# Performance work log

Hardware: AMD Instinct MI355X
Metric: run time of the kernel (lower is better)

The kernel has to match this reference:

```python
import jax, jax.numpy as jnp
import numpy as np

B, S1, S2, H = 8, 2048, 2048, 1024

def setup_inputs() -> dict:
    key = jax.random.key(0)
    k1, k2, k3, k4, k5, k6 = jax.random.split(key, 6)
    value = jax.random.normal(k1, (B, S1, H), dtype=jnp.float32)
    key_t = jax.random.normal(k2, (B, S2, H), dtype=jnp.float32)
    query = jax.random.normal(k3, (B, S1, H), dtype=jnp.float32)
    mask = jax.random.randint(k4, (B, S1, S2), 0, 2).astype(jnp.bool_)
    # Linear(hidden, hidden) params, torch default init scale
    bound = 1.0 / np.sqrt(H)
    W = jax.random.uniform(k5, (H, H), minval=-bound, maxval=bound, dtype=jnp.float32)
    b = jax.random.uniform(k6, (H,), minval=-bound, maxval=bound, dtype=jnp.float32)
    return {"value": value, "key": key_t, "query": query, "mask": mask, "W": W, "b": b}

def reference(value, key, query, mask, W, b):
    # q_proj = query @ W^T + b  (torch Linear)
    q_proj = jnp.einsum('bqh,oh->bqo', query, W) + b            # [B,S1,H]
    attn = jnp.einsum('bqh,bkh->bqk', q_proj, key)               # [B,S1,S2]
    attn = jnp.where(mask, -jnp.inf, attn)
    attn = jnp.transpose(attn, (0, 2, 1))                        # [B,S2,S1]
    weights = jax.nn.softmax(attn, axis=-1)                      # softmax over S1
    context = jnp.einsum('bks,bsh->bkh', weights, value)         # [B,S2,H]
    return context, weights
```

## Files before the change

### kernel.cpp

```cpp
#include <hip/hip_runtime.h>

#define B_  8
#define S1_ 2048
#define S2_ 2048
#define H_  1024

typedef unsigned short u16;
typedef __attribute__((ext_vector_type(8))) short short8;
typedef __attribute__((ext_vector_type(4))) float f32x4;

__device__ __forceinline__ float b2f(u16 u) {
  union { unsigned int i; float f; } v; v.i = ((unsigned int)u) << 16; return v.f;
}
__device__ __forceinline__ u16 f2b(float f) {
  union { float f; unsigned int i; } v; v.f = f;
  unsigned int r = v.i + 0x7fffu + ((v.i >> 16) & 1u);
  return (u16)(r >> 16);
}

__device__ __forceinline__ int swz(int row, int kk) {
  return (row * 32 + kk) ^ (((row >> 1) & 3) << 3);
}

__device__ __forceinline__ void cvt8_split(float4 va, float4 vb, short8* hi, short8* lo) {
  float x[8] = {va.x, va.y, va.z, va.w, vb.x, vb.y, vb.z, vb.w};
  short8 h, l;
#pragma unroll
  for (int e = 0; e < 8; ++e) {
    u16 hb = f2b(x[e]);
    h[e] = (short)hb;
    l[e] = (short)f2b(x[e] - b2f(hb));
  }
  *hi = h; *lo = l;
}
__device__ __forceinline__ short8 cvt8(float4 va, float4 vb) {
  float x[8] = {va.x, va.y, va.z, va.w, vb.x, vb.y, vb.z, vb.w};
  short8 h;
#pragma unroll
  for (int e = 0; e < 8; ++e) h[e] = (short)f2b(x[e]);
  return h;
}

__device__ __forceinline__ void g2l16(const void* g, void* lds) {
  __builtin_amdgcn_global_load_lds(
      (const __attribute__((address_space(1))) unsigned int*)g,
      (__attribute__((address_space(3))) unsigned int*)lds, 16, 0, 0);
}

template<bool ADD_BIAS, bool DO_MASK, bool SPLIT, bool OUTSPLIT>
__global__ __launch_bounds__(256)
void gemm_bf(const u16* __restrict__ Ahi, const u16* __restrict__ Alo, long sA, int lda,
             const u16* __restrict__ Bhi, const u16* __restrict__ Blo, long sB, int ldb,
             const float* __restrict__ bias,
             const int* __restrict__ mask, long sMask, int mask_ld,
             float* __restrict__ Cf, u16* __restrict__ Chi, u16* __restrict__ Clo,
             long sC, int ldc, int K)
{
  __shared__ __align__(16) union {
    u16 tile[SPLIT ? 4 : 2][128 * 32];
    unsigned char m[128][128];
  } sh;

  const int t    = threadIdx.x;
  const int lane = t & 63;
  const int wv   = t >> 6;
  const int wm   = wv >> 1, wn = wv & 1;
  const int batch = blockIdx.z;
  const int m0 = blockIdx.x * 128;
  const int n0 = blockIdx.y * 128;

  const u16* Ah = Ahi + (long)batch * sA + (long)m0 * lda;
  const u16* Bh = Bhi + (long)batch * sB + (long)n0 * ldb;
  const u16* Al = SPLIT ? (Alo + (long)batch * sA + (long)m0 * lda) : nullptr;
  const u16* Bl = SPLIT ? (Blo + (long)batch * sB + (long)n0 * ldb) : nullptr;

  f32x4 acc[4][4];
#pragma unroll
  for (int i = 0; i < 4; ++i)
#pragma unroll
    for (int j = 0; j < 4; ++j)
      acc[i][j] = (f32x4){0.f, 0.f, 0.f, 0.f};

  const int fr = lane & 15;
  const int kg = lane >> 4;

  int srow[2], soff[2], sdst[2];
#pragma unroll
  for (int half = 0; half < 2; ++half) {
    int c = half * 256 + wv * 64 + lane;
    int row = c >> 2;
    srow[half] = row;
    soff[half] = (((c & 3) ^ ((row >> 1) & 3)) * 8);
    sdst[half] = (half * 256 + wv * 64) * 8;
  }

  for (int kc = 0; kc < K; kc += 32) {
    __syncthreads();
#pragma unroll
    for (int half = 0; half < 2; ++half) {
      const int ga = srow[half] * lda + kc + soff[half];
      const int gb = srow[half] * ldb + kc + soff[half];
      g2l16(Ah + ga, &sh.tile[0][sdst[half]]);
      g2l16(Bh + gb, &sh.tile[1][sdst[half]]);
      if (SPLIT) {
        g2l16(Al + ga, &sh.tile[2][sdst[half]]);
        g2l16(Bl + gb, &sh.tile[3][sdst[half]]);
      }
    }
    __syncthreads();

    short8 afh[4], bfh[4];
#pragma unroll
    for (int i = 0; i < 4; ++i)
      afh[i] = *(const short8*)&sh.tile[0][swz(wm * 64 + i * 16 + fr, kg * 8)];
#pragma unroll
    for (int j = 0; j < 4; ++j)
      bfh[j] = *(const short8*)&sh.tile[1][swz(wn * 64 + j * 16 + fr, kg * 8)];

    if (SPLIT) {
      short8 afl[4], bfl[4];
#pragma unroll
      for (int i = 0; i < 4; ++i)
        afl[i] = *(const short8*)&sh.tile[2][swz(wm * 64 + i * 16 + fr, kg * 8)];
#pragma unroll
      for (int j = 0; j < 4; ++j)
        bfl[j] = *(const short8*)&sh.tile[3][swz(wn * 64 + j * 16 + fr, kg * 8)];
#pragma unroll
      for (int i = 0; i < 4; ++i)
#pragma unroll
        for (int j = 0; j < 4; ++j) {
          acc[i][j] = __builtin_amdgcn_mfma_f32_16x16x32_bf16(afh[i], bfh[j], acc[i][j], 0, 0, 0);
          acc[i][j] = __builtin_amdgcn_mfma_f32_16x16x32_bf16(afh[i], bfl[j], acc[i][j], 0, 0, 0);
          acc[i][j] = __builtin_amdgcn_mfma_f32_16x16x32_bf16(afl[i], bfh[j], acc[i][j], 0, 0, 0);
        }
    } else {
#pragma unroll
      for (int i = 0; i < 4; ++i)
#pragma unroll
        for (int j = 0; j < 4; ++j)
          acc[i][j] = __builtin_amdgcn_mfma_f32_16x16x32_bf16(afh[i], bfh[j], acc[i][j], 0, 0, 0);
    }
  }

  if (DO_MASK) {
    __syncthreads();
    const int* mb = mask + (long)batch * sMask;
#pragma unroll
    for (int it = 0; it < 16; ++it) {
      int ql = it * 8 + (t >> 5);
      int kl = (t & 31) * 4;
      int4 mv = *(const int4*)(mb + (long)(n0 + ql) * mask_ld + (m0 + kl));
      sh.m[kl + 0][ql] = (unsigned char)(mv.x != 0);
      sh.m[kl + 1][ql] = (unsigned char)(mv.y != 0);
      sh.m[kl + 2][ql] = (unsigned char)(mv.z != 0);
      sh.m[kl + 3][ql] = (unsigned char)(mv.w != 0);
    }
    __syncthreads();
  }

  float bv[4];
  if (ADD_BIAS) {
#pragma unroll
    for (int j = 0; j < 4; ++j)
      bv[j] = bias[n0 + wn * 64 + j * 16 + fr];
  }

#pragma unroll
  for (int i = 0; i < 4; ++i) {
#pragma unroll
    for (int r = 0; r < 4; ++r) {
      int row = wm * 64 + i * 16 + (lane >> 4) * 4 + r;
      long gro = (long)batch * sC + (long)(m0 + row) * ldc + n0;
#pragma unroll
      for (int j = 0; j < 4; ++j) {
        int col = wn * 64 + j * 16 + fr;
        float v = acc[i][j][r];
        if (ADD_BIAS) v += bv[j];
        if (OUTSPLIT) {
          u16 hb = f2b(v);
          Chi[gro + col] = hb;
          Clo[gro + col] = f2b(v - b2f(hb));
        } else {
          if (DO_MASK && sh.m[row][col]) v = -1e30f;
          Cf[gro + col] = v;
        }
      }
    }
  }
}

template<bool ADD_BIAS, bool DO_MASK, bool SPLIT, bool BTR>
__global__ __launch_bounds__(256)
void gemm_k(const float* __restrict__ A, long sA,
            const float* __restrict__ B, long sB, int ldb,
            const float* __restrict__ bias,
            const int* __restrict__ mask, long sMask, int mask_ld,
            float* __restrict__ C, long sC, int ldc, int K)
{
  __shared__ __align__(16) union {
    u16 tile[SPLIT ? 4 : 2][128 * 32];
    unsigned char m[128][128];
  } sh;

  const int t    = threadIdx.x;
  const int lane = t & 63;
  const int wv   = t >> 6;
  const int wm   = wv >> 1, wn = wv & 1;
  const int batch = blockIdx.z;
  const int m0 = blockIdx.x * 128;
  const int n0 = blockIdx.y * 128;

  const float* Ab = A + (long)batch * sA + (long)m0 * K;
  const float* Bb = B + (long)batch * sB + (BTR ? (long)n0 : (long)n0 * ldb);

  f32x4 acc[4][4];
#pragma unroll
  for (int i = 0; i < 4; ++i)
#pragma unroll
    for (int j = 0; j < 4; ++j)
      acc[i][j] = (f32x4){0.f, 0.f, 0.f, 0.f};

  const int c0 = t,       r0 = c0 >> 2, o0 = (c0 & 3) * 8;
  const int c1 = t + 256, r1 = c1 >> 2, o1 = (c1 & 3) * 8;

  const int fr = lane & 15;
  const int kg = lane >> 4;

  for (int kc = 0; kc < K; kc += 32) {
    float4 a00 = *(const float4*)(Ab + (long)r0 * K + kc + o0);
    float4 a01 = *(const float4*)(Ab + (long)r0 * K + kc + o0 + 4);
    float4 a10 = *(const float4*)(Ab + (long)r1 * K + kc + o1);
    float4 a11 = *(const float4*)(Ab + (long)r1 * K + kc + o1 + 4);
    float4 bb[4];
    float btv[2][8];
    if (BTR) {
#pragma unroll
      for (int p = 0; p < 2; ++p)
#pragma unroll
        for (int e = 0; e < 8; ++e)
          btv[p][e] = Bb[(long)(kc + wv * 8 + e) * ldb + lane + p * 64];
    } else {
      bb[0] = *(const float4*)(Bb + (long)r0 * ldb + kc + o0);
      bb[1] = *(const float4*)(Bb + (long)r0 * ldb + kc + o0 + 4);
      bb[2] = *(const float4*)(Bb + (long)r1 * ldb + kc + o1);
      bb[3] = *(const float4*)(Bb + (long)r1 * ldb + kc + o1 + 4);
    }
    __syncthreads();

    if (SPLIT) {
      short8 h, l;
      cvt8_split(a00, a01, &h, &l);
      *(short8*)&sh.tile[0][swz(r0, o0)] = h;  *(short8*)&sh.tile[2][swz(r0, o0)] = l;
      cvt8_split(a10, a11, &h, &l);
      *(short8*)&sh.tile[0][swz(r1, o1)] = h;  *(short8*)&sh.tile[2][swz(r1, o1)] = l;
      cvt8_split(bb[0], bb[1], &h, &l);
      *(short8*)&sh.tile[1][swz(r0, o0)] = h;  *(short8*)&sh.tile[3][swz(r0, o0)] = l;
      cvt8_split(bb[2], bb[3], &h, &l);
      *(short8*)&sh.tile[1][swz(r1, o1)] = h;  *(short8*)&sh.tile[3][swz(r1, o1)] = l;
    } else {
      *(short8*)&sh.tile[0][swz(r0, o0)] = cvt8(a00, a01);
      *(short8*)&sh.tile[0][swz(r1, o1)] = cvt8(a10, a11);
      if (BTR) {
#pragma unroll
        for (int p = 0; p < 2; ++p) {
          short8 h;
#pragma unroll
          for (int e = 0; e < 8; ++e) h[e] = (short)f2b(btv[p][e]);
          *(short8*)&sh.tile[1][swz(lane + p * 64, wv * 8)] = h;
        }
      } else {
        *(short8*)&sh.tile[1][swz(r0, o0)] = cvt8(bb[0], bb[1]);
        *(short8*)&sh.tile[1][swz(r1, o1)] = cvt8(bb[2], bb[3]);
      }
    }
    __syncthreads();

    short8 afh[4], bfh[4];
#pragma unroll
    for (int i = 0; i < 4; ++i)
      afh[i] = *(const short8*)&sh.tile[0][swz(wm * 64 + i * 16 + fr, kg * 8)];
#pragma unroll
    for (int j = 0; j < 4; ++j)
      bfh[j] = *(const short8*)&sh.tile[1][swz(wn * 64 + j * 16 + fr, kg * 8)];

    if (SPLIT) {
      short8 afl[4], bfl[4];
#pragma unroll
      for (int i = 0; i < 4; ++i)
        afl[i] = *(const short8*)&sh.tile[2][swz(wm * 64 + i * 16 + fr, kg * 8)];
#pragma unroll
      for (int j = 0; j < 4; ++j)
        bfl[j] = *(const short8*)&sh.tile[3][swz(wn * 64 + j * 16 + fr, kg * 8)];
#pragma unroll
      for (int i = 0; i < 4; ++i)
#pragma unroll
        for (int j = 0; j < 4; ++j) {
          acc[i][j] = __builtin_amdgcn_mfma_f32_16x16x32_bf16(afh[i], bfh[j], acc[i][j], 0, 0, 0);
          acc[i][j] = __builtin_amdgcn_mfma_f32_16x16x32_bf16(afh[i], bfl[j], acc[i][j], 0, 0, 0);
          acc[i][j] = __builtin_amdgcn_mfma_f32_16x16x32_bf16(afl[i], bfh[j], acc[i][j], 0, 0, 0);
        }
    } else {
#pragma unroll
      for (int i = 0; i < 4; ++i)
#pragma unroll
        for (int j = 0; j < 4; ++j)
          acc[i][j] = __builtin_amdgcn_mfma_f32_16x16x32_bf16(afh[i], bfh[j], acc[i][j], 0, 0, 0);
    }
  }

  if (DO_MASK) {
    __syncthreads();
    const int* mb = mask + (long)batch * sMask;
#pragma unroll
    for (int it = 0; it < 16; ++it) {
      int ql = it * 8 + (t >> 5);
      int kl = (t & 31) * 4;
      int4 mv = *(const int4*)(mb + (long)(n0 + ql) * mask_ld + (m0 + kl));
      sh.m[kl + 0][ql] = (unsigned char)(mv.x != 0);
      sh.m[kl + 1][ql] = (unsigned char)(mv.y != 0);
      sh.m[kl + 2][ql] = (unsigned char)(mv.z != 0);
      sh.m[kl + 3][ql] = (unsigned char)(mv.w != 0);
    }
    __syncthreads();
  }

  float bv[4];
  if (ADD_BIAS) {
#pragma unroll
    for (int j = 0; j < 4; ++j)
      bv[j] = bias[n0 + wn * 64 + j * 16 + fr];
  }

#pragma unroll
  for (int i = 0; i < 4; ++i) {
#pragma unroll
    for (int r = 0; r < 4; ++r) {
      int row = wm * 64 + i * 16 + (lane >> 4) * 4 + r;
      long gro = (long)batch * sC + (long)(m0 + row) * ldc + n0;
#pragma unroll
      for (int j = 0; j < 4; ++j) {
        int col = wn * 64 + j * 16 + fr;
        float v = acc[i][j][r];
        if (ADD_BIAS) v += bv[j];
        if (DO_MASK && sh.m[row][col]) v = -1e30f;
        C[gro + col] = v;
      }
    }
  }
}

__global__ __launch_bounds__(256)
void conv_split(const float* __restrict__ in, u16* __restrict__ hi, u16* __restrict__ lo)
{
  long i = ((long)blockIdx.x * 256 + threadIdx.x) * 8;
  float4 v0 = *(const float4*)(in + i);
  float4 v1 = *(const float4*)(in + i + 4);
  short8 h, l;
  cvt8_split(v0, v1, &h, &l);
  *(short8*)(hi + i) = h;
  *(short8*)(lo + i) = l;
}

__global__ __launch_bounds__(256)
void transpose_conv(const float* __restrict__ v, u16* __restrict__ vt)
{
  __shared__ u16 tl[64][66];
  const int b  = blockIdx.z;
  const int s0 = blockIdx.x * 64, h0 = blockIdx.y * 64;
  const int tr = threadIdx.x >> 4;
  const int tc = (threadIdx.x & 15) * 4;
  const float* vb = v + ((long)b * S1_ + s0) * H_ + h0;
#pragma unroll
  for (int q = 0; q < 4; ++q) {
    int r = tr + q * 16;
    float4 x = *(const float4*)(vb + (long)r * H_ + tc);
    tl[r][tc + 0] = f2b(x.x); tl[r][tc + 1] = f2b(x.y);
    tl[r][tc + 2] = f2b(x.z); tl[r][tc + 3] = f2b(x.w);
  }
  __syncthreads();
  u16* ob = vt + ((long)b * H_ + h0) * S1_ + s0;
#pragma unroll
  for (int q = 0; q < 4; ++q) {
    int hr = tr + q * 16;
    unsigned int w0 = (unsigned int)tl[tc + 0][hr] | ((unsigned int)tl[tc + 1][hr] << 16);
    unsigned int w1 = (unsigned int)tl[tc + 2][hr] | ((unsigned int)tl[tc + 3][hr] << 16);
    uint2 w = {w0, w1};
    *(uint2*)(ob + (long)hr * S1_ + tc) = w;
  }
}

__global__ __launch_bounds__(256)
void softmax_rows(float* __restrict__ scores, u16* __restrict__ wbf)
{
  const long row = blockIdx.x;
  float* p = scores + row * (long)S1_;
  const int t = threadIdx.x;
  const int lane = t & 63, wv = t >> 6;

  float4 v0 = *(const float4*)(p + t * 8);
  float4 v1 = *(const float4*)(p + t * 8 + 4);
  float x[8] = {v0.x, v0.y, v0.z, v0.w, v1.x, v1.y, v1.z, v1.w};

  float m = x[0];
#pragma unroll
  for (int q = 1; q < 8; ++q) m = fmaxf(m, x[q]);
#pragma unroll
  for (int o = 32; o; o >>= 1) m = fmaxf(m, __shfl_xor(m, o));
  __shared__ float rb[4], sb[4];
  if (lane == 0) rb[wv] = m;
  __syncthreads();
  m = fmaxf(fmaxf(rb[0], rb[1]), fmaxf(rb[2], rb[3]));

  float e[8]; float s = 0.f;
#pragma unroll
  for (int q = 0; q < 8; ++q) { e[q] = __expf(x[q] - m); s += e[q]; }
#pragma unroll
  for (int o = 32; o; o >>= 1) s += __shfl_xor(s, o);
  if (lane == 0) sb[wv] = s;
  __syncthreads();
  s = sb[0] + sb[1] + sb[2] + sb[3];
  float inv = 1.f / s;

  float w[8];
#pragma unroll
  for (int q = 0; q < 8; ++q) w[q] = e[q] * inv;
  float4 o0 = {w[0], w[1], w[2], w[3]};
  float4 o1 = {w[4], w[5], w[6], w[7]};
  *(float4*)(p + t * 8)     = o0;
  *(float4*)(p + t * 8 + 4) = o1;

  if (wbf != nullptr) {
    short8 hb;
#pragma unroll
    for (int q = 0; q < 8; ++q) hb[q] = (short)f2b(w[q]);
    *(short8*)(wbf + row * (long)S1_ + t * 8) = hb;
  }
}

extern "C" void kernel_launch(void* const* d_in, const int* in_sizes, int n_in,
                              void* d_out, int out_size, void* d_ws, size_t ws_size,
                              hipStream_t stream)
{
  const float* value = (const float*)d_in[0];
  const float* key   = (const float*)d_in[1];
  const float* query = (const float*)d_in[2];
  const int*   mask  = (const int*)d_in[3];
  const float* W     = (const float*)d_in[4];
  const float* bias  = (const float*)d_in[5];

  float* ctx = (float*)d_out;
  float* wts = ctx + (size_t)B_ * S2_ * H_;

  dim3 blk(256);
  const size_t MB = 1024ull * 1024ull;

  if (ws_size >= 132 * MB && d_ws != nullptr) {
    u16* pjhi = (u16*)ctx;
    u16* pjlo = (u16*)ctx + (size_t)B_ * S1_ * H_;

    char* ws = (char*)d_ws;
    u16* khi = (u16*)(ws);
    u16* klo = (u16*)(ws + 32 * MB);
    u16* wbf = (u16*)(ws);
    u16* qhi = (u16*)(ws + 64 * MB);
    u16* qlo = (u16*)(ws + 96 * MB);
    u16* vT  = (u16*)(ws + 64 * MB);
    u16* whi = (u16*)(ws + 128 * MB);
    u16* wlo = (u16*)(ws + 130 * MB);

    conv_split<<<dim3((B_ * S1_ * H_) / 2048), blk, 0, stream>>>(query, qhi, qlo);
    conv_split<<<dim3((B_ * S2_ * H_) / 2048), blk, 0, stream>>>(key, khi, klo);
    conv_split<<<dim3((H_ * H_) / 2048), blk, 0, stream>>>(W, whi, wlo);

    gemm_bf<true, false, true, true><<<dim3((B_ * S1_) / 128, H_ / 128, 1), blk, 0, stream>>>(
        qhi, qlo, 0, H_, whi, wlo, 0, H_, bias,
        nullptr, 0, 0, nullptr, pjhi, pjlo, 0, H_, H_);

    transpose_conv<<<dim3(S1_ / 64, H_ / 64, B_), blk, 0, stream>>>(value, vT);

    gemm_bf<false, true, true, false><<<dim3(S2_ / 128, S1_ / 128, B_), blk, 0, stream>>>(
        khi, klo, (long)S2_ * H_, H_, pjhi, pjlo, (long)S1_ * H_, H_, nullptr,
        mask, (long)S1_ * S2_, S2_, wts, nullptr, nullptr, (long)S2_ * S1_, S1_, H_);

    softmax_rows<<<dim3(B_ * S2_), blk, 0, stream>>>(wts, wbf);

    gemm_bf<false, false, false, false><<<dim3(S2_ / 128, H_ / 128, B_), blk, 0, stream>>>(
        wbf, nullptr, (long)S2_ * S1_, S1_, vT, nullptr, (long)H_ * S1_, S1_, nullptr,
        nullptr, 0, 0, ctx, nullptr, nullptr, (long)S2_ * H_, H_, S1_);
  } else {
    float* qproj = ctx;

    gemm_k<true, false, true, false><<<dim3((B_ * S1_) / 128, H_ / 128, 1), blk, 0, stream>>>(
        query, 0, W, 0, H_, bias, nullptr, 0, 0, qproj, 0, H_, H_);

    gemm_k<false, true, true, false><<<dim3(S2_ / 128, S1_ / 128, B_), blk, 0, stream>>>(
        key, (long)S2_ * H_, qproj, (long)S1_ * H_, H_, nullptr,
        mask, (long)S1_ * S2_, S2_, wts, (long)S2_ * S1_, S1_, H_);

    softmax_rows<<<dim3(B_ * S2_), blk, 0, stream>>>(wts, nullptr);

    gemm_k<false, false, false, true><<<dim3(S2_ / 128, H_ / 128, B_), blk, 0, stream>>>(
        wts, (long)S2_ * S1_, value, (long)S1_ * H_, H_, nullptr,
        nullptr, 0, 0, ctx, (long)S2_ * H_, H_, S1_);
  }
}
```

Baseline: 950.4 us.

## Double-buffer LDS tiles, swizzle block order across XCDs, raise MFMA priority

Adds a second LDS tile buffer so the global-to-LDS load of the next K slice is issued before the MFMAs on the current slice, with one barrier per iteration instead of two. Remaps the linear block id so consecutive blocks land on the same XCD chunk, aiming for better L2 reuse. Wraps the MFMA loops in s_setprio to favour compute waves. Doubling LDS use may lower occupancy. The remap assumes the total block count divides by 8.

```diff
diff --git a/kernel.cpp b/kernel.cpp
--- a/kernel.cpp
+++ b/kernel.cpp
@@ -56,8 +56,9 @@
              float* __restrict__ Cf, u16* __restrict__ Chi, u16* __restrict__ Clo,
              long sC, int ldc, int K)
 {
+  constexpr int NP = SPLIT ? 4 : 2;
   __shared__ __align__(16) union {
-    u16 tile[SPLIT ? 4 : 2][128 * 32];
+    u16 tile[2][NP][128 * 32];
     unsigned char m[128][128];
   } sh;
 
@@ -65,9 +66,17 @@
   const int lane = t & 63;
   const int wv   = t >> 6;
   const int wm   = wv >> 1, wn = wv & 1;
-  const int batch = blockIdx.z;
-  const int m0 = blockIdx.x * 128;
-  const int n0 = blockIdx.y * 128;
+
+  const int nbx = gridDim.x, nby = gridDim.y;
+  const int id  = blockIdx.x + nbx * (blockIdx.y + nby * blockIdx.z);
+  const int cpx = (nbx * nby * (int)gridDim.z) >> 3;
+  const int sid = (id & 7) * cpx + (id >> 3);
+  const int bx  = sid % nbx;
+  const int rem = sid / nbx;
+  const int by  = rem % nby;
+  const int batch = rem / nby;
+  const int m0 = bx * 128;
+  const int n0 = by * 128;
 
   const u16* Ah = Ahi + (long)batch * sA + (long)m0 * lda;
   const u16* Bh = Bhi + (long)batch * sB + (long)n0 * ldb;
@@ -94,37 +103,44 @@
     sdst[half] = (half * 256 + wv * 64) * 8;
   }
 
-  for (int kc = 0; kc < K; kc += 32) {
-    __syncthreads();
+  auto STAGE = [&](int kc, int bufi) {
 #pragma unroll
     for (int half = 0; half < 2; ++half) {
       const int ga = srow[half] * lda + kc + soff[half];
       const int gb = srow[half] * ldb + kc + soff[half];
-      g2l16(Ah + ga, &sh.tile[0][sdst[half]]);
-      g2l16(Bh + gb, &sh.tile[1][sdst[half]]);
+      g2l16(Ah + ga, &sh.tile[bufi][0][sdst[half]]);
+      g2l16(Bh + gb, &sh.tile[bufi][1][sdst[half]]);
       if (SPLIT) {
-        g2l16(Al + ga, &sh.tile[2][sdst[half]]);
-        g2l16(Bl + gb, &sh.tile[3][sdst[half]]);
+        g2l16(Al + ga, &sh.tile[bufi][2][sdst[half]]);
+        g2l16(Bl + gb, &sh.tile[bufi][3][sdst[half]]);
       }
     }
-    __syncthreads();
+  };
+
+  STAGE(0, 0);
+  __syncthreads();
+  int cur = 0;
+
+  for (int kc = 0; kc < K; kc += 32) {
+    if (kc + 32 < K) STAGE(kc + 32, cur ^ 1);
 
     short8 afh[4], bfh[4];
 #pragma unroll
     for (int i = 0; i < 4; ++i)
-      afh[i] = *(const short8*)&sh.tile[0][swz(wm * 64 + i * 16 + fr, kg * 8)];
+      afh[i] = *(const short8*)&sh.tile[cur][0][swz(wm * 64 + i * 16 + fr, kg * 8)];
 #pragma unroll
     for (int j = 0; j < 4; ++j)
-      bfh[j] = *(const short8*)&sh.tile[1][swz(wn * 64 + j * 16 + fr, kg * 8)];
+      bfh[j] = *(const short8*)&sh.tile[cur][1][swz(wn * 64 + j * 16 + fr, kg * 8)];
 
     if (SPLIT) {
       short8 afl[4], bfl[4];
 #pragma unroll
       for (int i = 0; i < 4; ++i)
-        afl[i] = *(const short8*)&sh.tile[2][swz(wm * 64 + i * 16 + fr, kg * 8)];
+        afl[i] = *(const short8*)&sh.tile[cur][2][swz(wm * 64 + i * 16 + fr, kg * 8)];
 #pragma unroll
       for (int j = 0; j < 4; ++j)
-        bfl[j] = *(const short8*)&sh.tile[3][swz(wn * 64 + j * 16 + fr, kg * 8)];
+        bfl[j] = *(const short8*)&sh.tile[cur][3][swz(wn * 64 + j * 16 + fr, kg * 8)];
+      __builtin_amdgcn_s_setprio(1);
 #pragma unroll
       for (int i = 0; i < 4; ++i)
 #pragma unroll
@@ -133,17 +149,22 @@
           acc[i][j] = __builtin_amdgcn_mfma_f32_16x16x32_bf16(afh[i], bfl[j], acc[i][j], 0, 0, 0);
           acc[i][j] = __builtin_amdgcn_mfma_f32_16x16x32_bf16(afl[i], bfh[j], acc[i][j], 0, 0, 0);
         }
+      __builtin_amdgcn_s_setprio(0);
     } else {
+      __builtin_amdgcn_s_setprio(1);
 #pragma unroll
       for (int i = 0; i < 4; ++i)
 #pragma unroll
         for (int j = 0; j < 4; ++j)
           acc[i][j] = __builtin_amdgcn_mfma_f32_16x16x32_bf16(afh[i], bfh[j], acc[i][j], 0, 0, 0);
-    }
+      __builtin_amdgcn_s_setprio(0);
+    }
+
+    __syncthreads();
+    cur ^= 1;
   }
 
   if (DO_MASK) {
-    __syncthreads();
     const int* mb = mask + (long)batch * sMask;
 #pragma unroll
     for (int it = 0; it < 16; ++it) {
```

New measurement: 878.1 us. 7.6% less time.
